# Kernel tuning notes

Hardware: AMD Instinct MI355X
Metric: run time of the kernel (lower is better)

Reference implementation:

```python
import jax, jax.numpy as jnp
import numpy as np

H = 16  # num_attention_heads


def setup_inputs() -> dict:
    key = jax.random.key(0)
    k1, k2, k3 = jax.random.split(key, 3)
    B, S, E = 2, 2048, 1024
    return {
        "hidden_states": jax.random.normal(k1, (B, S, E), dtype=jnp.float32),
        "W_attn": jax.random.normal(k2, (E, 3 * E), dtype=jnp.float32) * 0.02,
        "b_attn": jnp.zeros((3 * E,), dtype=jnp.float32),
        "W_proj": jax.random.normal(k3, (E, E), dtype=jnp.float32) * 0.02,
        "b_proj": jnp.zeros((E,), dtype=jnp.float32),
    }


def reference(hidden_states, W_attn, b_attn, W_proj, b_proj):
    B, S, E = hidden_states.shape
    hd = E // H
    # Conv1D: x @ W + b -> [B, S, 3E]
    qkv = hidden_states @ W_attn + b_attn
    # Faithful to module: _split_heads with 3*head_dim FIRST, then split q/k/v.
    # i.e. per-head slice of size 3*hd is [q_h | k_h | v_h] (interleaved layout).
    qkv = qkv.reshape(B, S, H, 3 * hd).transpose(0, 2, 1, 3)  # [B, H, S, 3*hd]
    q, k, v = jnp.split(qkv, 3, axis=-1)                      # each [B, H, S, hd]
    # scores, scaled by sqrt(head_dim) (value.size(-1) ** 0.5)
    scores = jnp.einsum("bhqd,bhkd->bhqk", q, k) / jnp.asarray(hd, q.dtype) ** 0.5
    # causal mask via where with masked_bias = -10000.0 (not -inf), as in module
    causal = jnp.tril(jnp.ones((S, S), dtype=bool))
    scores = jnp.where(causal, scores, jnp.asarray(-10000.0, scores.dtype))
    attn_weights = jax.nn.softmax(scores, axis=-1)  # dropout p=0 -> identity
    attn_out = jnp.einsum("bhqk,bhkd->bhqd", attn_weights, v)
    attn_out = attn_out.transpose(0, 2, 1, 3).reshape(B, S, E)  # merge heads
    return attn_out @ W_proj + b_proj
```

## Files before the change

### kernel.cpp

```cpp
#include <hip/hip_runtime.h>
#include <hip/hip_bf16.h>


typedef __attribute__((ext_vector_type(4))) float f32x4;
typedef __attribute__((ext_vector_type(16))) float f32x16;
typedef __attribute__((ext_vector_type(8))) short short8;
typedef __attribute__((ext_vector_type(2))) unsigned int uint2v;

#define AS1 __attribute__((address_space(1)))
#define AS3 __attribute__((address_space(3)))

__device__ __forceinline__ void load_lds16(const void* g, void* l) {
    __builtin_amdgcn_global_load_lds((const AS1 void*)g, (AS3 void*)l, 16, 0, 0);
}

__device__ __forceinline__ unsigned short f2bf(float f) {
    union { float f; unsigned int u; } v; v.f = f;
    unsigned int r = v.u + 0x7FFFu + ((v.u >> 16) & 1u);
    return (unsigned short)(r >> 16);
}

__device__ __forceinline__ int cvt_pk_bf16(float lo, float hi) {
    int r;
    asm("v_cvt_pk_bf16_f32 %0, %1, %2" : "=v"(r) : "v"(lo), "v"(hi));
    return r;
}

__device__ __forceinline__ float fexp2(float x) {
    float r;
    asm("v_exp_f32 %0, %1" : "=v"(r) : "v"(x));
    return r;
}

__device__ __forceinline__ void transpose_tile(
    const float* __restrict__ W, unsigned short* __restrict__ Wt,
    int K, int N, int bx, int by, int t) {
    __shared__ float tile[32][33];
    int k0 = by * 32, n0 = bx * 32;
    int r = t >> 3, c = (t & 7) * 4;
    float4 v = *(const float4*)&W[(size_t)(k0 + r) * N + n0 + c];
    tile[r][c] = v.x; tile[r][c + 1] = v.y; tile[r][c + 2] = v.z; tile[r][c + 3] = v.w;
    __syncthreads();
    int n = t >> 3; int kk = (t & 7) * 4;
    ushort4 o;
    o.x = f2bf(tile[kk + 0][n]);
    o.y = f2bf(tile[kk + 1][n]);
    o.z = f2bf(tile[kk + 2][n]);
    o.w = f2bf(tile[kk + 3][n]);
    *(ushort4*)&Wt[(size_t)(n0 + n) * K + k0 + kk] = o;
}

__global__ __launch_bounds__(256) void prep(
    const float* __restrict__ hs, unsigned short* __restrict__ Xb,
    const float* __restrict__ W_attn, unsigned short* __restrict__ WaT,
    const float* __restrict__ W_proj, unsigned short* __restrict__ WpT) {
    int bid = blockIdx.x, t = threadIdx.x;
    if (bid < 4096) {
        int i = (bid * 256 + t) * 4;
        float4 v = *(const float4*)(hs + i);
        ushort4 o;
        o.x = f2bf(v.x); o.y = f2bf(v.y); o.z = f2bf(v.z); o.w = f2bf(v.w);
        *(ushort4*)(Xb + i) = o;
    } else if (bid < 7168) {
        int r = bid - 4096;
        transpose_tile(W_attn, WaT, 1024, 3072, r % 96, r / 96, t);
    } else {
        int r = bid - 7168;
        transpose_tile(W_proj, WpT, 1024, 1024, r % 32, r / 32, t);
    }
}

__global__ __launch_bounds__(512, 6) void gemm_qkv(
    const unsigned short* __restrict__ A,
    const unsigned short* __restrict__ Bt,
    const float* __restrict__ bias,
    unsigned short* __restrict__ qk, unsigned short* __restrict__ Vt,
    int M, int N, int K) {
    __shared__ unsigned short Sh[2][8192];
    unsigned short* Tb = &Sh[0][0];
    const int t = threadIdx.x, wave = t >> 6, lane = t & 63;
    const int l15 = lane & 15, quad = lane >> 4;
    const int m0 = blockIdx.y * 128, n0 = blockIdx.x * 128;
    const int sw = wave & 3;
    const bool isB = wave >= 4;
    const int srow = sw * 32 + (lane >> 2);
    const int sch = (lane & 3) * 8;
    const unsigned short* G0 = isB ? (Bt + (size_t)(n0 + srow) * K + sch)
                                   : (A + (size_t)(m0 + srow) * K + sch);
    const int stOff = (isB ? 4096 : 0) + sw * 1024;
    const int wr = wave >> 1, wc = wave & 1;
    f32x4 acc[2][4] = {};
    const int NSTEP = K / 32;
    load_lds16(G0, &Sh[0][stOff]);
    load_lds16(G0 + (size_t)16 * K, &Sh[0][stOff + 512]);
    for (int kt = 0; kt < NSTEP; ++kt) {
        const int cur = kt & 1;
        const unsigned short* As = &Sh[cur][0];
        const unsigned short* Bs = &Sh[cur][4096];
        __syncthreads();
        if (kt + 1 < NSTEP) {
            const int k1 = (kt + 1) * 32;
            load_lds16(G0 + k1, &Sh[cur ^ 1][stOff]);
            load_lds16(G0 + k1 + (size_t)16 * K, &Sh[cur ^ 1][stOff + 512]);
        }
        short8 af[2], bf[4];
#pragma unroll
        for (int i = 0; i < 2; ++i)
            af[i] = *(const short8*)&As[(wr * 32 + i * 16 + l15) * 32 + quad * 8];
#pragma unroll
        for (int i = 0; i < 4; ++i)
            bf[i] = *(const short8*)&Bs[(wc * 64 + i * 16 + l15) * 32 + quad * 8];
        __builtin_amdgcn_s_setprio(1);
#pragma unroll
        for (int mt = 0; mt < 2; ++mt)
#pragma unroll
            for (int nt = 0; nt < 4; ++nt)
                acc[mt][nt] = __builtin_amdgcn_mfma_f32_16x16x32_bf16(af[mt], bf[nt], acc[mt][nt], 0, 0, 0);
        __builtin_amdgcn_s_setprio(0);
    }
    __syncthreads();
    const int rem = n0 % 192;
#pragma unroll
    for (int mt = 0; mt < 2; ++mt) {
        int mrow = m0 + wr * 32 + mt * 16 + quad * 4;
#pragma unroll
        for (int nt = 0; nt < 4; ++nt) {
            int col = n0 + wc * 64 + nt * 16 + l15;
            float bv = bias[col];
            int h = col / 192;
            int j = col - h * 192;
            if (j < 128) {
                float sc = (j < 64) ? 0.18033688011f : 1.0f;
#pragma unroll
                for (int r = 0; r < 4; ++r)
                    qk[(size_t)(mrow + r) * 2048 + h * 128 + j] = f2bf((acc[mt][nt][r] + bv) * sc);
            } else {
                int d = j - 128;
                int s_local = wr * 32 + mt * 16 + quad * 4;
                ushort4 pk;
                pk.x = f2bf(acc[mt][nt][0] + bv);
                pk.y = f2bf(acc[mt][nt][1] + bv);
                pk.z = f2bf(acc[mt][nt][2] + bv);
                pk.w = f2bf(acc[mt][nt][3] + bv);
                *(ushort4*)&Tb[d * 136 + s_local] = pk;
            }
        }
    }
    if (rem != 0) {
        __syncthreads();
        int vhalf = (rem == 64) ? 1 : 0;
        int h = (n0 + vhalf * 64) / 192;
        int b = m0 >> 11;
        unsigned short* vbase = Vt + ((size_t)(b * 16 + h) * 64) * 2048 + (m0 & 2047);
        int drow = t >> 4, ch = (t & 15) * 8;
#pragma unroll
        for (int rr = 0; rr < 2; ++rr) {
            int d = rr * 32 + drow;
            *(uint4*)(vbase + (size_t)d * 2048 + ch) = *(const uint4*)&Tb[d * 136 + ch];
        }
    }
}

__global__ __launch_bounds__(512, 4) void gemm_proj(
    const unsigned short* __restrict__ A,
    const unsigned short* __restrict__ Bt,
    const float* __restrict__ bias,
    float* __restrict__ C, int M, int N, int K) {
    __shared__ unsigned short Sh[2][6144];
    const int t = threadIdx.x, wave = t >> 6, lane = t & 63;
    const int l15 = lane & 15, quad = lane >> 4;
    const int m0 = blockIdx.y * 128, n0 = blockIdx.x * 64;
    const int sw = wave & 3;
    const bool isB = wave >= 4;
    const int srow = isB ? (sw * 16 + (lane >> 2)) : (sw * 32 + (lane >> 2));
    const int sch = (lane & 3) * 8;
    const unsigned short* G0 = isB ? (Bt + (size_t)(n0 + srow) * K + sch)
                                   : (A + (size_t)(m0 + srow) * K + sch);
    const int stOff = isB ? (4096 + sw * 512) : (sw * 1024);
    const int wr = wave >> 1, wc = wave & 1;
    f32x4 acc[2][2] = {};
    const int NSTEP = K / 32;
    load_lds16(G0, &Sh[0][stOff]);
    if (!isB) load_lds16(G0 + (size_t)16 * K, &Sh[0][stOff + 512]);
    for (int kt = 0; kt < NSTEP; ++kt) {
        const int cur = kt & 1;
        const unsigned short* As = &Sh[cur][0];
        const unsigned short* Bs = &Sh[cur][4096];
        __syncthreads();
        if (kt + 1 < NSTEP) {
            const int k1 = (kt + 1) * 32;
            load_lds16(G0 + k1, &Sh[cur ^ 1][stOff]);
            if (!isB) load_lds16(G0 + k1 + (size_t)16 * K, &Sh[cur ^ 1][stOff + 512]);
        }
        short8 af[2], bf[2];
#pragma unroll
        for (int i = 0; i < 2; ++i)
            af[i] = *(const short8*)&As[(wr * 32 + i * 16 + l15) * 32 + quad * 8];
#pragma unroll
        for (int i = 0; i < 2; ++i)
            bf[i] = *(const short8*)&Bs[(wc * 32 + i * 16 + l15) * 32 + quad * 8];
        __builtin_amdgcn_s_setprio(1);
#pragma unroll
        for (int mt = 0; mt < 2; ++mt)
#pragma unroll
            for (int nt = 0; nt < 2; ++nt)
                acc[mt][nt] = __builtin_amdgcn_mfma_f32_16x16x32_bf16(af[mt], bf[nt], acc[mt][nt], 0, 0, 0);
        __builtin_amdgcn_s_setprio(0);
    }
#pragma unroll
    for (int mt = 0; mt < 2; ++mt) {
        int mrow = m0 + wr * 32 + mt * 16 + quad * 4;
#pragma unroll
        for (int nt = 0; nt < 2; ++nt) {
            int col = n0 + wc * 32 + nt * 16 + l15;
            float bv = bias[col];
#pragma unroll
            for (int r = 0; r < 4; ++r)
                C[(size_t)(mrow + r) * N + col] = acc[mt][nt][r] + bv;
        }
    }
}

__global__ __launch_bounds__(512, 4) void attn5(
    const unsigned short* __restrict__ qk,
    const unsigned short* __restrict__ Vt,
    unsigned short* __restrict__ out) {
    const int S = 2048;
    __shared__ unsigned short Sh[16384];
    const int t = threadIdx.x, wave = t >> 6, lane = t & 63;
    const int l31 = lane & 31, half = lane >> 5;
    const int g = wave >> 2, gw = wave & 3;
    const int bid = blockIdx.x;
    const int qt = (bid < 256) ? (15 - (bid >> 5)) : ((bid - 256) >> 5);
    const int bh = bid & 31;
    const int b = bh >> 4, h = bh & 15;
    const unsigned short* qkb = qk + (size_t)b * S * 2048 + h * 128;
    const unsigned short* vtb = Vt + (size_t)bh * 64 * 2048;

    const int q0 = qt * 128 + gw * 32;
    short8 qf[4];
#pragma unroll
    for (int km = 0; km < 4; ++km)
        qf[km] = *(const short8*)(qkb + (size_t)(q0 + l31) * 2048 + km * 16 + half * 8);

    f32x16 o[2] = {};
    float lrun = 0.f;

    const int srow = t >> 3, ch16 = t & 7;
    const int swz = srow * 64 + ((ch16 ^ (srow & 7)) * 8);
    const int KTP = qt + 1;

    uint4 kE = *(const uint4*)(qkb + (size_t)srow * 2048 + 64 + ch16 * 8);
    uint4 kO = *(const uint4*)(qkb + (size_t)(64 + srow) * 2048 + 64 + ch16 * 8);
    uint4 vE = *(const uint4*)(vtb + (size_t)srow * 2048 + ch16 * 8);
    uint4 vO = *(const uint4*)(vtb + (size_t)srow * 2048 + 64 + ch16 * 8);

    const int qmax = q0 + 31;
    const int ksw = l31 & 7;
    int chs[4];
#pragma unroll
    for (int km = 0; km < 4; ++km)
        chs[km] = ((km * 2 + half) ^ ksw) * 8;
    const int krow = l31 * 64;
    const unsigned short* Ksg = Sh + (g ? 4096 : 0);
    const unsigned short* Vsg = Sh + 8192 + (g ? 4096 : 0);

    for (int p = 0; p < KTP; ++p) {
        *(uint4*)&Sh[swz] = kE;
        *(uint4*)&Sh[4096 + swz] = kO;
        *(uint4*)&Sh[8192 + swz] = vE;
        *(uint4*)&Sh[12288 + swz] = vO;
        __syncthreads();
        if (p + 1 < KTP) {
            const int k2 = (2 * p + 2) * 64, k3 = k2 + 64;
            kE = *(const uint4*)(qkb + (size_t)(k2 + srow) * 2048 + 64 + ch16 * 8);
            kO = *(const uint4*)(qkb + (size_t)(k3 + srow) * 2048 + 64 + ch16 * 8);
            vE = *(const uint4*)(vtb + (size_t)srow * 2048 + k2 + ch16 * 8);
            vO = *(const uint4*)(vtb + (size_t)srow * 2048 + k3 + ch16 * 8);
        }
        const int kb = (2 * p + g) * 64;
        if (kb <= qmax) {
            f32x16 s[2] = {};
            __builtin_amdgcn_s_setprio(1);
#pragma unroll
            for (int nt = 0; nt < 2; ++nt)
#pragma unroll
                for (int km = 0; km < 4; ++km) {
                    short8 kf = *(const short8*)&Ksg[nt * 2048 + krow + chs[km]];
                    s[nt] = __builtin_amdgcn_mfma_f32_32x32x16_bf16(kf, qf[km], s[nt], 0, 0, 0);
                }
            __builtin_amdgcn_s_setprio(0);

            if (kb + 63 > q0) {
#pragma unroll
                for (int nt = 0; nt < 2; ++nt)
#pragma unroll
                    for (int r = 0; r < 16; ++r) {
                        int kg = kb + nt * 32 + (r & 3) + 8 * (r >> 2) + 4 * half;
                        if (kg > q0 + l31) s[nt][r] = -1e30f;
                    }
            }

            int gd[2][4][2];
            float a0 = 0.f;
#pragma unroll
            for (int nt = 0; nt < 2; ++nt)
#pragma unroll
                for (int gg = 0; gg < 4; ++gg) {
                    float e0 = fexp2(s[nt][4 * gg + 0]);
                    float e1 = fexp2(s[nt][4 * gg + 1]);
                    float e2 = fexp2(s[nt][4 * gg + 2]);
                    float e3 = fexp2(s[nt][4 * gg + 3]);
                    a0 += (e0 + e1) + (e2 + e3);
                    gd[nt][gg][0] = cvt_pk_bf16(e0, e1);
                    gd[nt][gg][1] = cvt_pk_bf16(e2, e3);
                }
            lrun += a0;

            short8 paf[4];
#pragma unroll
            for (int km = 0; km < 4; ++km) {
                const int nt = km >> 1, m = km & 1;
                uint2v w0 = __builtin_amdgcn_permlane32_swap(
                    (unsigned)gd[nt][2 * m][0], (unsigned)gd[nt][2 * m + 1][0], false, false);
                uint2v w1 = __builtin_amdgcn_permlane32_swap(
                    (unsigned)gd[nt][2 * m][1], (unsigned)gd[nt][2 * m + 1][1], false, false);
                int4 v = {(int)w0[0], (int)w1[0], (int)w0[1], (int)w1[1]};
                paf[km] = __builtin_bit_cast(short8, v);
            }

            __builtin_amdgcn_s_setprio(1);
#pragma unroll
            for (int nt2 = 0; nt2 < 2; ++nt2)
#pragma unroll
                for (int km = 0; km < 4; ++km) {
                    short8 vf = *(const short8*)&Vsg[nt2 * 2048 + krow + chs[km]];
                    o[nt2] = __builtin_amdgcn_mfma_f32_32x32x16_bf16(paf[km], vf, o[nt2], 0, 0, 0);
                }
            __builtin_amdgcn_s_setprio(0);
        }
        __syncthreads();
    }

    float* Lf = (float*)Sh;
    const int cidx = gw * 64 + lane;
    if (g == 1) {
        float* dst = Lf + cidx * 17;
#pragma unroll
        for (int r = 0; r < 16; ++r) dst[r] = o[0][r];
        dst[16] = lrun;
    }
    __syncthreads();
    float lsum = lrun;
    if (g == 0) {
        const float* src = Lf + cidx * 17;
#pragma unroll
        for (int r = 0; r < 16; ++r) o[0][r] += src[r];
        lsum += src[16];
    }
    __syncthreads();
    if (g == 1) {
        float* dst = Lf + cidx * 16;
#pragma unroll
        for (int r = 0; r < 16; ++r) dst[r] = o[1][r];
    }
    __syncthreads();
    if (g == 0) {
        const float* src = Lf + cidx * 16;
#pragma unroll
        for (int r = 0; r < 16; ++r) o[1][r] += src[r];
        float tot = lsum + __shfl_xor(lsum, 32);
        unsigned short* ob = out + (size_t)b * S * 1024 + h * 64;
#pragma unroll
        for (int r = 0; r < 16; ++r) {
            int ql = (r & 3) + 8 * (r >> 2) + 4 * half;
            float inv = 1.0f / __shfl(tot, ql);
            size_t row = (size_t)(q0 + ql) * 1024;
            ob[row + l31] = f2bf(o[0][r] * inv);
            ob[row + 32 + l31] = f2bf(o[1][r] * inv);
        }
    }
}

extern "C" void kernel_launch(void* const* d_in, const int* in_sizes, int n_in,
                              void* d_out, int out_size, void* d_ws, size_t ws_size,
                              hipStream_t stream) {
    const float* hs     = (const float*)d_in[0];
    const float* W_attn = (const float*)d_in[1];
    const float* b_attn = (const float*)d_in[2];
    const float* W_proj = (const float*)d_in[3];
    const float* b_proj = (const float*)d_in[4];
    float* out = (float*)d_out;

    const int B = 2, S = 2048, E = 1024;
    const int M = B * S;
    const int N3 = 3 * E;

    unsigned short* Xb  = (unsigned short*)d_ws;
    unsigned short* WaT = Xb + (size_t)M * E;
    unsigned short* WpT = WaT + (size_t)N3 * E;
    unsigned short* qkb = WpT + (size_t)E * E;
    unsigned short* Vt  = qkb + (size_t)M * 2048;
    unsigned short* ao  = Vt + (size_t)M * E;

    prep<<<dim3(8192), 256, 0, stream>>>(hs, Xb, W_attn, WaT, W_proj, WpT);

    gemm_qkv<<<dim3(N3 / 128, M / 128), 512, 0, stream>>>(Xb, WaT, b_attn, qkb, Vt, M, N3, E);

    attn5<<<dim3(512), 512, 0, stream>>>(qkb, Vt, ao);

    gemm_proj<<<dim3(E / 64, M / 128), 512, 0, stream>>>(ao, WpT, b_proj, out, M, E, E);
}
```

Baseline: 167.2 us.

## Double-buffer attention K/V tiles with direct global-to-LDS loads

The attention kernel now stages K and V tiles through two LDS buffers and fills them with global_load_lds DMA instead of loading into registers and then storing to LDS. The swizzle moves to the global source address. This removes one of the two barriers per iteration and frees the staging registers. It doubles LDS use per block, which may cut occupancy, and it relies on global_load_lds completing before the next barrier. The loop-top __syncthreads may not wait for outstanding vmcnt unless the compiler inserts that wait.

```diff
diff --git a/kernel.cpp b/kernel.cpp
--- a/kernel.cpp
+++ b/kernel.cpp
@@ -221,12 +221,12 @@
     }
 }
 
-__global__ __launch_bounds__(512, 4) void attn5(
+__global__ __launch_bounds__(512, 4) void attn6(
     const unsigned short* __restrict__ qk,
     const unsigned short* __restrict__ Vt,
     unsigned short* __restrict__ out) {
     const int S = 2048;
-    __shared__ unsigned short Sh[16384];
+    __shared__ unsigned short Sh[2][16384];
     const int t = threadIdx.x, wave = t >> 6, lane = t & 63;
     const int l31 = lane & 31, half = lane >> 5;
     const int g = wave >> 2, gw = wave & 3;
@@ -246,14 +246,17 @@
     f32x16 o[2] = {};
     float lrun = 0.f;
 
-    const int srow = t >> 3, ch16 = t & 7;
-    const int swz = srow * 64 + ((ch16 ^ (srow & 7)) * 8);
+    const int srow = t >> 3, c8 = t & 7;
+    const int gsw = ((c8 ^ (srow & 7)) * 8);
+    const int ldst = wave * 512;
+    const unsigned short* kSrc = qkb + (size_t)srow * 2048 + 64 + gsw;
+    const unsigned short* vSrc = vtb + (size_t)srow * 2048 + gsw;
     const int KTP = qt + 1;
 
-    uint4 kE = *(const uint4*)(qkb + (size_t)srow * 2048 + 64 + ch16 * 8);
-    uint4 kO = *(const uint4*)(qkb + (size_t)(64 + srow) * 2048 + 64 + ch16 * 8);
-    uint4 vE = *(const uint4*)(vtb + (size_t)srow * 2048 + ch16 * 8);
-    uint4 vO = *(const uint4*)(vtb + (size_t)srow * 2048 + 64 + ch16 * 8);
+    load_lds16(kSrc, &Sh[0][ldst]);
+    load_lds16(kSrc + (size_t)64 * 2048, &Sh[0][4096 + ldst]);
+    load_lds16(vSrc, &Sh[0][8192 + ldst]);
+    load_lds16(vSrc + 64, &Sh[0][12288 + ldst]);
 
     const int qmax = q0 + 31;
     const int ksw = l31 & 7;
@@ -262,87 +265,87 @@
     for (int km = 0; km < 4; ++km)
         chs[km] = ((km * 2 + half) ^ ksw) * 8;
     const int krow = l31 * 64;
-    const unsigned short* Ksg = Sh + (g ? 4096 : 0);
-    const unsigned short* Vsg = Sh + 8192 + (g ? 4096 : 0);
+    const int gOff = g ? 4096 : 0;
 
     for (int p = 0; p < KTP; ++p) {
-        *(uint4*)&Sh[swz] = kE;
-        *(uint4*)&Sh[4096 + swz] = kO;
-        *(uint4*)&Sh[8192 + swz] = vE;
-        *(uint4*)&Sh[12288 + swz] = vO;
+        const int cur = p & 1;
         __syncthreads();
         if (p + 1 < KTP) {
-            const int k2 = (2 * p + 2) * 64, k3 = k2 + 64;
-            kE = *(const uint4*)(qkb + (size_t)(k2 + srow) * 2048 + 64 + ch16 * 8);
-            kO = *(const uint4*)(qkb + (size_t)(k3 + srow) * 2048 + 64 + ch16 * 8);
-            vE = *(const uint4*)(vtb + (size_t)srow * 2048 + k2 + ch16 * 8);
-            vO = *(const uint4*)(vtb + (size_t)srow * 2048 + k3 + ch16 * 8);
+            const int k2 = (2 * p + 2) * 64;
+            unsigned short* nb = &Sh[cur ^ 1][0];
+            load_lds16(kSrc + (size_t)k2 * 2048, nb + ldst);
+            load_lds16(kSrc + (size_t)(k2 + 64) * 2048, nb + 4096 + ldst);
+            load_lds16(vSrc + k2, nb + 8192 + ldst);
+            load_lds16(vSrc + k2 + 64, nb + 12288 + ldst);
         }
         const int kb = (2 * p + g) * 64;
-        if (kb <= qmax) {
-            f32x16 s[2] = {};
-            __builtin_amdgcn_s_setprio(1);
+        if (kb > qmax) continue;
+
+        const unsigned short* Ksg = &Sh[cur][gOff];
+        const unsigned short* Vsg = &Sh[cur][8192 + gOff];
+
+        f32x16 s[2] = {};
+        __builtin_amdgcn_s_setprio(1);
+#pragma unroll
+        for (int nt = 0; nt < 2; ++nt)
+#pragma unroll
+            for (int km = 0; km < 4; ++km) {
+                short8 kf = *(const short8*)&Ksg[nt * 2048 + krow + chs[km]];
+                s[nt] = __builtin_amdgcn_mfma_f32_32x32x16_bf16(kf, qf[km], s[nt], 0, 0, 0);
+            }
+        __builtin_amdgcn_s_setprio(0);
+
+        if (kb + 63 > q0) {
 #pragma unroll
             for (int nt = 0; nt < 2; ++nt)
 #pragma unroll
-                for (int km = 0; km < 4; ++km) {
-                    short8 kf = *(const short8*)&Ksg[nt * 2048 + krow + chs[km]];
-                    s[nt] = __builtin_amdgcn_mfma_f32_32x32x16_bf16(kf, qf[km], s[nt], 0, 0, 0);
+                for (int r = 0; r < 16; ++r) {
+                    int kg = kb + nt * 32 + (r & 3) + 8 * (r >> 2) + 4 * half;
+                    if (kg > q0 + l31) s[nt][r] = -1e30f;
                 }
-            __builtin_amdgcn_s_setprio(0);
-
-            if (kb + 63 > q0) {
-#pragma unroll
-                for (int nt = 0; nt < 2; ++nt)
-#pragma unroll
-                    for (int r = 0; r < 16; ++r) {
-                        int kg = kb + nt * 32 + (r & 3) + 8 * (r >> 2) + 4 * half;
-                        if (kg > q0 + l31) s[nt][r] = -1e30f;
-                    }
+        }
+
+        int gd[2][4][2];
+        float a0 = 0.f;
+#pragma unroll
+        for (int nt = 0; nt < 2; ++nt)
+#pragma unroll
+            for (int gg = 0; gg < 4; ++gg) {
+                float e0 = fexp2(s[nt][4 * gg + 0]);
+                float e1 = fexp2(s[nt][4 * gg + 1]);
+                float e2 = fexp2(s[nt][4 * gg + 2]);
+                float e3 = fexp2(s[nt][4 * gg + 3]);
+                a0 += (e0 + e1) + (e2 + e3);
+                gd[nt][gg][0] = cvt_pk_bf16(e0, e1);
+                gd[nt][gg][1] = cvt_pk_bf16(e2, e3);
             }
-
-            int gd[2][4][2];
-            float a0 = 0.f;
-#pragma unroll
-            for (int nt = 0; nt < 2; ++nt)
-#pragma unroll
-                for (int gg = 0; gg < 4; ++gg) {
-                    float e0 = fexp2(s[nt][4 * gg + 0]);
-                    float e1 = fexp2(s[nt][4 * gg + 1]);
-                    float e2 = fexp2(s[nt][4 * gg + 2]);
-                    float e3 = fexp2(s[nt][4 * gg + 3]);
-                    a0 += (e0 + e1) + (e2 + e3);
-                    gd[nt][gg][0] = cvt_pk_bf16(e0, e1);
-                    gd[nt][gg][1] = cvt_pk_bf16(e2, e3);
-                }
-            lrun += a0;
-
-            short8 paf[4];
+        lrun += a0;
+
+        short8 paf[4];
+#pragma unroll
+        for (int km = 0; km < 4; ++km) {
+            const int nt = km >> 1, m = km & 1;
+            uint2v w0 = __builtin_amdgcn_permlane32_swap(
+                (unsigned)gd[nt][2 * m][0], (unsigned)gd[nt][2 * m + 1][0], false, false);
+            uint2v w1 = __builtin_amdgcn_permlane32_swap(
+                (unsigned)gd[nt][2 * m][1], (unsigned)gd[nt][2 * m + 1][1], false, false);
+            int4 v = {(int)w0[0], (int)w1[0], (int)w0[1], (int)w1[1]};
+            paf[km] = __builtin_bit_cast(short8, v);
+        }
+
+        __builtin_amdgcn_s_setprio(1);
+#pragma unroll
+        for (int nt2 = 0; nt2 < 2; ++nt2)
 #pragma unroll
             for (int km = 0; km < 4; ++km) {
-                const int nt = km >> 1, m = km & 1;
-                uint2v w0 = __builtin_amdgcn_permlane32_swap(
-                    (unsigned)gd[nt][2 * m][0], (unsigned)gd[nt][2 * m + 1][0], false, false);
-                uint2v w1 = __builtin_amdgcn_permlane32_swap(
-                    (unsigned)gd[nt][2 * m][1], (unsigned)gd[nt][2 * m + 1][1], false, false);
-                int4 v = {(int)w0[0], (int)w1[0], (int)w0[1], (int)w1[1]};
-                paf[km] = __builtin_bit_cast(short8, v);
+                short8 vf = *(const short8*)&Vsg[nt2 * 2048 + krow + chs[km]];
+                o[nt2] = __builtin_amdgcn_mfma_f32_32x32x16_bf16(paf[km], vf, o[nt2], 0, 0, 0);
             }
-
-            __builtin_amdgcn_s_setprio(1);
-#pragma unroll
-            for (int nt2 = 0; nt2 < 2; ++nt2)
-#pragma unroll
-                for (int km = 0; km < 4; ++km) {
-                    short8 vf = *(const short8*)&Vsg[nt2 * 2048 + krow + chs[km]];
-                    o[nt2] = __builtin_amdgcn_mfma_f32_32x32x16_bf16(paf[km], vf, o[nt2], 0, 0, 0);
-                }
-            __builtin_amdgcn_s_setprio(0);
-        }
-        __syncthreads();
-    }
-
-    float* Lf = (float*)Sh;
+        __builtin_amdgcn_s_setprio(0);
+    }
+    __syncthreads();
+
+    float* Lf = (float*)&Sh[0][0];
     const int cidx = gw * 64 + lane;
     if (g == 1) {
         float* dst = Lf + cidx * 17;
@@ -407,7 +410,7 @@
 
     gemm_qkv<<<dim3(N3 / 128, M / 128), 512, 0, stream>>>(Xb, WaT, b_attn, qkb, Vt, M, N3, E);
 
-    attn5<<<dim3(512), 512, 0, stream>>>(qkb, Vt, ao);
+    attn6<<<dim3(512), 512, 0, stream>>>(qkb, Vt, ao);
 
     gemm_proj<<<dim3(E / 64, M / 128), 512, 0, stream>>>(ao, WpT, b_proj, out, M, E, E);
 }
```

After: 164.6 us. No clear change (-1.6%).
